# Kernel tuning notes

Hardware: AMD Instinct MI355X
Metric: run time of the kernel (lower is better)

The kernel has to match this reference:

```python
import jax, jax.numpy as jnp
import numpy as np

IN_DIM = 4096
OUT_DIM = 4096
NUM_ACTIVE = 32
BATCH = 4096


def _make_mask(key):
    # exactly NUM_ACTIVE ones per row (matches create_mask's row invariant)
    r = jax.random.uniform(key, (OUT_DIM, IN_DIM))
    cols = jnp.argsort(r, axis=1)[:, :NUM_ACTIVE]           # [out, num_active]
    rows = jnp.arange(OUT_DIM)[:, None]
    mask = jnp.zeros((OUT_DIM, IN_DIM), dtype=jnp.int32)
    return mask.at[rows, cols].set(1)


def setup_inputs() -> dict:
    key = jax.random.key(0)
    k1, k2, k3, k4 = jax.random.split(key, 4)
    x = jax.random.normal(k1, (BATCH, IN_DIM), dtype=jnp.float32)
    # xavier-uniform-ish weight
    bound_w = float(np.sqrt(6.0 / (IN_DIM + OUT_DIM)))
    weight = jax.random.uniform(k2, (OUT_DIM, IN_DIM), dtype=jnp.float32,
                                minval=-bound_w, maxval=bound_w)
    bound_b = 1.0 / float(np.sqrt(NUM_ACTIVE))
    bias = jax.random.uniform(k3, (OUT_DIM,), dtype=jnp.float32,
                              minval=-bound_b, maxval=bound_b)
    mask = _make_mask(k4)
    return {"x": x, "weight": weight, "bias": bias, "mask": mask}


def reference(x, weight, bias, mask):
    # effective weight = weight * fixed binary mask; y = x @ W_eff^T - bias
    w_eff = weight * mask.astype(weight.dtype)              # [out, in]
    return jnp.einsum('bi,oi->bo', x, w_eff) - bias
```

## Files before the change

### kernel.cpp

```cpp
#include <hip/hip_runtime.h>
#include <stdint.h>

#define IN_DIM  4096
#define OUT_DIM 4096
#define BATCH   4096
#define NACT    32

typedef float          f32x4  __attribute__((ext_vector_type(4)));
typedef unsigned short u16x4  __attribute__((ext_vector_type(4)));

__device__ inline unsigned short f2bf(float f) {
    unsigned u = __float_as_uint(f);
    u += 0x7FFF + ((u >> 16) & 1);
    return (unsigned short)(u >> 16);
}

__global__ __launch_bounds__(256)
void prep_kernel(const float* __restrict__ weight,
                 const int*   __restrict__ mask,
                 const float* __restrict__ x,
                 int*         __restrict__ idx_tab,
                 float*       __restrict__ w_tab,
                 unsigned short* __restrict__ xT) {
    __shared__ float tile[64][65];
    int* scan = (int*)&tile[0][0];
    const int t = threadIdx.x;

    if (blockIdx.x < OUT_DIM) {
        const int o = blockIdx.x;
        const int* mrow = mask + (size_t)o * IN_DIM;
        const int  base = t * 16;

        int m[16];
        const int4* m4 = (const int4*)(mrow + base);
        #pragma unroll
        for (int j = 0; j < 4; ++j) {
            int4 v = m4[j];
            m[j*4+0] = v.x; m[j*4+1] = v.y; m[j*4+2] = v.z; m[j*4+3] = v.w;
        }
        int c = 0;
        #pragma unroll
        for (int j = 0; j < 16; ++j) c += (m[j] != 0);

        scan[t] = c;
        __syncthreads();
        for (int off = 1; off < 256; off <<= 1) {
            int add = (t >= off) ? scan[t - off] : 0;
            __syncthreads();
            scan[t] += add;
            __syncthreads();
        }
        int pos = scan[t] - c;
        for (int j = 0; j < 16; ++j) {
            if (m[j] != 0) {
                int idx = base + j;
                idx_tab[o * NACT + pos] = idx;
                w_tab [o * NACT + pos] = weight[(size_t)o * IN_DIM + idx];
                ++pos;
            }
        }
    } else {
        const int q  = blockIdx.x - OUT_DIM;
        const int bi = q & 63;
        const int bj = q >> 6;
        {
            const int c  = (t & 15) * 4;
            const int r0 = t >> 4;
            #pragma unroll
            for (int p = 0; p < 4; ++p) {
                int r = r0 + p * 16;
                float4 v = *(const float4*)(x + (size_t)(bi*64 + r) * IN_DIM + bj*64 + c);
                tile[r][c+0] = v.x; tile[r][c+1] = v.y;
                tile[r][c+2] = v.z; tile[r][c+3] = v.w;
            }
        }
        __syncthreads();
        {
            const int b4 = (t & 15) * 4;
            const int j0 = t >> 4;
            #pragma unroll
            for (int p = 0; p < 4; ++p) {
                int j = j0 + p * 16;
                u16x4 v = { f2bf(tile[b4+0][j]), f2bf(tile[b4+1][j]),
                            f2bf(tile[b4+2][j]), f2bf(tile[b4+3][j]) };
                *(u16x4*)(xT + (size_t)(bj*64 + j) * BATCH + bi*64 + b4) = v;
            }
        }
    }
}

__global__ __launch_bounds__(128)
void spmm_kernel(const unsigned short* __restrict__ xT,
                 const int*   __restrict__ idx_tab,
                 const float* __restrict__ w_tab,
                 const float* __restrict__ bias,
                 float*       __restrict__ out) {
    const int t   = threadIdx.x;
    const int bid = blockIdx.x;
    const int v    = (bid & 7) * 512 + (bid >> 3);
    const int slab = v >> 8;
    const int ot   = v & 255;
    const int o0   = ot * 16;
    const int b0   = slab * 256;
    const int bl   = t * 2;

    const unsigned* xTd = (const unsigned*)xT;
    const int bl2 = (b0 >> 1) + t;

    float acc0[16], acc1[16];
    #pragma unroll 2
    for (int o = 0; o < 16; ++o) {
        const int*   ip = idx_tab + (size_t)(o0 + o) * NACT;
        const float* wp = w_tab   + (size_t)(o0 + o) * NACT;
        float a00 = 0.f, a01 = 0.f, a10 = 0.f, a11 = 0.f;
        #pragma unroll
        for (int k = 0; k < NACT; k += 2) {
            int r0 = __builtin_amdgcn_readfirstlane(ip[k]);
            int r1 = __builtin_amdgcn_readfirstlane(ip[k+1]);
            unsigned u0 = xTd[(size_t)r0 * (BATCH/2) + bl2];
            unsigned u1 = xTd[(size_t)r1 * (BATCH/2) + bl2];
            float x00 = __uint_as_float(u0 << 16);
            float x01 = __uint_as_float(u0 & 0xFFFF0000u);
            float x10 = __uint_as_float(u1 << 16);
            float x11 = __uint_as_float(u1 & 0xFFFF0000u);
            a00 = fmaf(wp[k],   x00, a00);
            a01 = fmaf(wp[k],   x01, a01);
            a10 = fmaf(wp[k+1], x10, a10);
            a11 = fmaf(wp[k+1], x11, a11);
        }
        const float bo = bias[o0 + o];
        acc0[o] = (a00 + a10) - bo;
        acc1[o] = (a01 + a11) - bo;
    }

    __shared__ float L[128 * 17];
    #pragma unroll
    for (int h = 0; h < 2; ++h) {
        if ((t >> 6) == h) {
            const int r = bl & 127;
            #pragma unroll
            for (int o = 0; o < 16; ++o) {
                L[(r + 0) * 17 + o] = acc0[o];
                L[(r + 1) * 17 + o] = acc1[o];
            }
        }
        __syncthreads();
        const int rr = t >> 2;
        const int c  = (t & 3) * 4;
        #pragma unroll
        for (int p = 0; p < 4; ++p) {
            int r = rr + p * 32;
            f32x4 rv = { L[r*17 + c+0], L[r*17 + c+1],
                         L[r*17 + c+2], L[r*17 + c+3] };
            __builtin_nontemporal_store(rv,
                (f32x4*)(out + (size_t)(b0 + h*128 + r) * OUT_DIM + o0 + c));
        }
        __syncthreads();
    }
}

__global__ __launch_bounds__(256)
void spmm_noT_kernel(const float* __restrict__ x,
                     const int*   __restrict__ idx_tab,
                     const float* __restrict__ w_tab,
                     const float* __restrict__ bias,
                     float*       __restrict__ out) {
    const int t   = threadIdx.x;
    const int bid = blockIdx.x;
    const int slab = bid >> 8;
    const int ot   = bid & 255;
    const int o0   = ot * 16;
    const int b    = slab * 256 + t;

    float acc[16];
    #pragma unroll 1
    for (int o = 0; o < 16; ++o) {
        const int*   ip = idx_tab + (size_t)(o0 + o) * NACT;
        const float* wp = w_tab   + (size_t)(o0 + o) * NACT;
        float a = 0.f;
        for (int k = 0; k < NACT; ++k)
            a = fmaf(wp[k], x[(size_t)b * IN_DIM + ip[k]], a);
        acc[o] = a - bias[o0 + o];
    }
    float* op = out + (size_t)b * OUT_DIM + o0;
    #pragma unroll
    for (int q = 0; q < 4; ++q) {
        float4 r; r.x = acc[q*4+0]; r.y = acc[q*4+1];
                  r.z = acc[q*4+2]; r.w = acc[q*4+3];
        *(float4*)(op + q*4) = r;
    }
}

__global__ __launch_bounds__(256)
void naive_kernel(const float* __restrict__ x,
                  const float* __restrict__ weight,
                  const float* __restrict__ bias,
                  const int*   __restrict__ mask,
                  float*       __restrict__ out) {
    const int o = blockIdx.x;
    const int t = threadIdx.x;
    __shared__ int   scan[256];
    __shared__ int   sidx[NACT];
    __shared__ float sw[NACT];

    const int* mrow = mask + (size_t)o * IN_DIM;
    const int  base = t * 16;
    int c = 0;
    #pragma unroll
    for (int j = 0; j < 16; ++j) c += (mrow[base + j] != 0);
    scan[t] = c;
    __syncthreads();
    for (int off = 1; off < 256; off <<= 1) {
        int add = (t >= off) ? scan[t - off] : 0;
        __syncthreads();
        scan[t] += add;
        __syncthreads();
    }
    int pos = scan[t] - c;
    for (int j = 0; j < 16; ++j) {
        if (mrow[base + j] != 0) {
            sidx[pos] = base + j;
            sw[pos]   = weight[(size_t)o * IN_DIM + base + j];
            ++pos;
        }
    }
    __syncthreads();
    const float bo = bias[o];
    for (int b = t; b < BATCH; b += 256) {
        float a = 0.f;
        #pragma unroll
        for (int k = 0; k < NACT; ++k)
            a = fmaf(sw[k], x[(size_t)b * IN_DIM + sidx[k]], a);
        out[(size_t)b * OUT_DIM + o] = a - bo;
    }
}

extern "C" void kernel_launch(void* const* d_in, const int* in_sizes, int n_in,
                              void* d_out, int out_size, void* d_ws, size_t ws_size,
                              hipStream_t stream) {
    const float* x      = (const float*)d_in[0];
    const float* weight = (const float*)d_in[1];
    const float* bias   = (const float*)d_in[2];
    const int*   mask   = (const int*)  d_in[3];
    float* out = (float*)d_out;

    const size_t TAB_BYTES  = (size_t)OUT_DIM * NACT * (sizeof(int) + sizeof(float));
    const size_t XT_BYTES   = (size_t)IN_DIM * BATCH * sizeof(unsigned short);
    const size_t NEED_FULL  = TAB_BYTES + XT_BYTES;

    if (ws_size >= NEED_FULL) {
        int*   idx_tab = (int*)d_ws;
        float* w_tab   = (float*)((char*)d_ws + (size_t)OUT_DIM * NACT * sizeof(int));
        unsigned short* xT = (unsigned short*)((char*)d_ws + TAB_BYTES);

        prep_kernel<<<OUT_DIM + (BATCH/64)*(IN_DIM/64), 256, 0, stream>>>(
            weight, mask, x, idx_tab, w_tab, xT);
        spmm_kernel<<<4096, 128, 0, stream>>>(xT, idx_tab, w_tab, bias, out);
    } else if (ws_size >= TAB_BYTES) {
        int*   idx_tab = (int*)d_ws;
        float* w_tab   = (float*)((char*)d_ws + (size_t)OUT_DIM * NACT * sizeof(int));
        prep_kernel<<<OUT_DIM, 256, 0, stream>>>(
            weight, mask, x, idx_tab, w_tab, (unsigned short*)nullptr);
        spmm_noT_kernel<<<4096, 256, 0, stream>>>(x, idx_tab, w_tab, bias, out);
    } else {
        naive_kernel<<<OUT_DIM, 256, 0, stream>>>(x, weight, bias, mask, out);
    }
}
```

Before: 91.47 us.

## Double-buffer gathered xT rows into LDS via async global_load_lds

The SpMM kernel now gathers the 16 selected xT rows per half-output into LDS with direct global-to-LDS loads, double-buffered so the next chunk's gather overlaps the FMAs on the current one. Previously each thread issued dependent per-element global loads with readfirstlane. The change adds two block barriers per chunk and manual vmcnt waits, and it reuses the LDS buffer for the output transpose.

```diff
diff --git a/kernel.cpp b/kernel.cpp
--- a/kernel.cpp
+++ b/kernel.cpp
@@ -13,6 +13,12 @@
     unsigned u = __float_as_uint(f);
     u += 0x7FFF + ((u >> 16) & 1);
     return (unsigned short)(u >> 16);
+}
+
+__device__ __forceinline__ void gload_lds16(const void* g, void* l) {
+    __builtin_amdgcn_global_load_lds(
+        (const __attribute__((address_space(1))) void*)g,
+        (__attribute__((address_space(3))) void*)l, 16, 0, 0);
 }
 
 __global__ __launch_bounds__(256)
@@ -96,44 +102,79 @@
                  const float* __restrict__ bias,
                  float*       __restrict__ out) {
     const int t   = threadIdx.x;
+    const int wv  = t >> 6;
+    const int l   = t & 63;
     const int bid = blockIdx.x;
     const int v    = (bid & 7) * 512 + (bid >> 3);
     const int slab = v >> 8;
     const int ot   = v & 255;
     const int o0   = ot * 16;
     const int b0   = slab * 256;
-    const int bl   = t * 2;
-
-    const unsigned* xTd = (const unsigned*)xT;
-    const int bl2 = (b0 >> 1) + t;
+
+    __shared__ uint buf[2][2048];
+
+    const int lane_half = l >> 5;
+    const int lane_in   = l & 31;
+    const char* gbase = (const char*)xT + (size_t)b0 * 2 + lane_in * 16;
+
+    float bv[16];
+    #pragma unroll
+    for (int o = 0; o < 16; ++o) bv[o] = bias[o0 + o];
 
     float acc0[16], acc1[16];
-    #pragma unroll 2
-    for (int o = 0; o < 16; ++o) {
-        const int*   ip = idx_tab + (size_t)(o0 + o) * NACT;
-        const float* wp = w_tab   + (size_t)(o0 + o) * NACT;
-        float a00 = 0.f, a01 = 0.f, a10 = 0.f, a11 = 0.f;
-        #pragma unroll
-        for (int k = 0; k < NACT; k += 2) {
-            int r0 = __builtin_amdgcn_readfirstlane(ip[k]);
-            int r1 = __builtin_amdgcn_readfirstlane(ip[k+1]);
-            unsigned u0 = xTd[(size_t)r0 * (BATCH/2) + bl2];
-            unsigned u1 = xTd[(size_t)r1 * (BATCH/2) + bl2];
-            float x00 = __uint_as_float(u0 << 16);
-            float x01 = __uint_as_float(u0 & 0xFFFF0000u);
-            float x10 = __uint_as_float(u1 << 16);
-            float x11 = __uint_as_float(u1 & 0xFFFF0000u);
-            a00 = fmaf(wp[k],   x00, a00);
-            a01 = fmaf(wp[k],   x01, a01);
-            a10 = fmaf(wp[k+1], x10, a10);
-            a11 = fmaf(wp[k+1], x11, a11);
-        }
-        const float bo = bias[o0 + o];
-        acc0[o] = (a00 + a10) - bo;
-        acc1[o] = (a01 + a11) - bo;
-    }
-
-    __shared__ float L[128 * 17];
+    float a0 = 0.f, a1 = 0.f;
+
+    {
+        const int* ip = idx_tab + (size_t)o0 * NACT;
+        #pragma unroll
+        for (int q = 0; q < 4; ++q) {
+            int i  = wv * 4 + q;
+            int r0 = ip[2*i];
+            int r1 = ip[2*i + 1];
+            int row = lane_half ? r1 : r0;
+            gload_lds16(gbase + ((size_t)row << 13), &buf[0][i * 256]);
+        }
+    }
+
+    #pragma unroll
+    for (int c = 0; c < 32; ++c) {
+        const int p = c & 1;
+        if (c < 31) {
+            const int cn = c + 1;
+            const int* ip = idx_tab + (size_t)(o0 + (cn >> 1)) * NACT + (cn & 1) * 16;
+            #pragma unroll
+            for (int q = 0; q < 4; ++q) {
+                int i  = wv * 4 + q;
+                int r0 = ip[2*i];
+                int r1 = ip[2*i + 1];
+                int row = lane_half ? r1 : r0;
+                gload_lds16(gbase + ((size_t)row << 13), &buf[p ^ 1][i * 256]);
+            }
+            asm volatile("s_waitcnt vmcnt(4)" ::: "memory");
+        } else {
+            asm volatile("s_waitcnt vmcnt(0)" ::: "memory");
+        }
+        __builtin_amdgcn_sched_barrier(0);
+        __builtin_amdgcn_s_barrier();
+
+        const float* wp = w_tab + (size_t)(o0 + (c >> 1)) * NACT + (c & 1) * 16;
+        if ((c & 1) == 0) { a0 = 0.f; a1 = 0.f; }
+        #pragma unroll
+        for (int j = 0; j < 16; ++j) {
+            uint u = buf[p][j * 128 + t];
+            float wj = wp[j];
+            a0 = fmaf(wj, __uint_as_float(u << 16),         a0);
+            a1 = fmaf(wj, __uint_as_float(u & 0xFFFF0000u), a1);
+        }
+        if (c & 1) {
+            acc0[c >> 1] = a0 - bv[c >> 1];
+            acc1[c >> 1] = a1 - bv[c >> 1];
+        }
+        __builtin_amdgcn_s_barrier();
+    }
+
+    float* L = (float*)&buf[0][0];
+    const int bl = t * 2;
     #pragma unroll
     for (int h = 0; h < 2; ++h) {
         if ((t >> 6) == h) {
@@ -146,14 +187,14 @@
         }
         __syncthreads();
         const int rr = t >> 2;
-        const int c  = (t & 3) * 4;
-        #pragma unroll
-        for (int p = 0; p < 4; ++p) {
-            int r = rr + p * 32;
-            f32x4 rv = { L[r*17 + c+0], L[r*17 + c+1],
-                         L[r*17 + c+2], L[r*17 + c+3] };
+        const int cc = (t & 3) * 4;
+        #pragma unroll
+        for (int pp = 0; pp < 4; ++pp) {
+            int r = rr + pp * 32;
+            f32x4 rv = { L[r*17 + cc+0], L[r*17 + cc+1],
+                         L[r*17 + cc+2], L[r*17 + cc+3] };
             __builtin_nontemporal_store(rv,
-                (f32x4*)(out + (size_t)(b0 + h*128 + r) * OUT_DIM + o0 + c));
+                (f32x4*)(out + (size_t)(b0 + h*128 + r) * OUT_DIM + o0 + cc));
         }
         __syncthreads();
     }
```

Measured after the change: 98.47 us. 1.08x slower.
